# Performance work log

Hardware: AMD Instinct MI355X
Metric: run time of the kernel (lower is better)

Reference implementation:

```python
import jax, jax.numpy as jnp
import numpy as np

DIM = 768
NUM_HEADS = 12
HEAD_DIM = DIM // NUM_HEADS
TIME_STEPS = 4
TAU_MEM = 2.0
THRESH = 1.0
NOISE_PROB = 0.01


def setup_inputs() -> dict:
    key = jax.random.key(0)
    ks = jax.random.split(key, 9)
    B, N = 8, 1024
    s = 1.0 / np.sqrt(DIM)
    inp = {"x": jax.random.normal(ks[0], (B, N, DIM), jnp.float32)}
    for i, nm in enumerate(["q", "k", "v", "o"]):
        inp["W" + nm] = jax.random.normal(ks[1 + i], (DIM, DIM), jnp.float32) * s
        inp["b" + nm] = jax.random.normal(ks[5 + i], (DIM,), jnp.float32) * 0.01
    return inp


def _lif_spikes(inp):
    """Multi-step LIF: constant input each step, leaky integrate, hard threshold,
    soft reset; aggregated spikes clamped to 1 (binary). Straight-through sigmoid
    surrogate keeps the op differentiable without changing forward values."""
    decay = jnp.exp(jnp.asarray(-1.0 / TAU_MEM, inp.dtype))

    def step(v, _):
        v = v * decay + inp
        sur = jax.nn.sigmoid(4.0 * (v - THRESH))
        hard = (v >= THRESH).astype(inp.dtype)
        spike = jax.lax.stop_gradient(hard - sur) + sur
        v = v - THRESH * spike
        return v, spike

    _, spikes = jax.lax.scan(step, jnp.zeros_like(inp), None, length=TIME_STEPS)
    # sum over time then clamp(max=1.0) -> binary aggregate spike map
    return jnp.minimum(spikes.sum(axis=0), 1.0)


def reference(x, Wq, bq, Wk, bk, Wv, bv, Wo, bo):
    B, N, C = x.shape
    q_lin = x @ Wq.T + bq
    k_lin = x @ Wk.T + bk
    v_lin = x @ Wv.T + bv

    s_q = _lif_spikes(q_lin)  # (B,N,C) binary
    s_k = _lif_spikes(k_lin)
    s_v = _lif_spikes(v_lin)

    # noise injection for fully-silent samples (deterministic key)
    silent = jnp.all(s_q == 0, axis=(1, 2)) & jnp.all(s_k == 0, axis=(1, 2))  # (B,)
    nk = jax.random.split(jax.random.key(42), 2)
    noise_q = (jax.random.uniform(nk[0], s_q.shape) < NOISE_PROB).astype(s_q.dtype)
    noise_k = (jax.random.uniform(nk[1], s_k.shape) < NOISE_PROB).astype(s_k.dtype)
    s_q = jnp.where(silent[:, None, None], jnp.maximum(s_q, noise_q), s_q)
    s_k = jnp.where(silent[:, None, None], jnp.maximum(s_k, noise_k), s_k)

    # (B,H,N,Dh)
    s_q = s_q.reshape(B, N, NUM_HEADS, HEAD_DIM).transpose(0, 2, 1, 3)
    s_k = s_k.reshape(B, N, NUM_HEADS, HEAD_DIM).transpose(0, 2, 1, 3)
    s_v = s_v.reshape(B, N, NUM_HEADS, HEAD_DIM).transpose(0, 2, 1, 3)

    # XNOR similarity: sum_d (1 - (q-k)^2) = Dh - |q| - |k| + 2 q.k  (exact, since
    # the broadcast form expands to the same polynomial; q,k binary so q^2=q)
    q2 = jnp.sum(s_q * s_q, axis=-1)  # (B,H,N)
    k2 = jnp.sum(s_k * s_k, axis=-1)  # (B,H,N)
    qk = jnp.einsum('bhnd,bhmd->bhnm', s_q, s_k)
    scores = HEAD_DIM - q2[..., :, None] - k2[..., None, :] + 2.0 * qk  # (B,H,N,N)

    attn = jax.nn.sigmoid(scores)
    out = jnp.einsum('bhnm,bhmd->bhnd', attn, s_v)  # (B,H,N,Dh)
    out = out.transpose(0, 2, 1, 3).reshape(B, N, C)
    return out @ Wo.T + bo
```

## Files before the change

kernel.cpp:

```cpp
#include <hip/hip_runtime.h>


typedef __attribute__((ext_vector_type(8))) short short8;
typedef __attribute__((ext_vector_type(4))) float f32x4;
typedef unsigned long long u64;

static __device__ __forceinline__ unsigned short f2bf(float f) {
  unsigned int u = __builtin_bit_cast(unsigned int, f);
  return (unsigned short)((u + 0x7FFFu + ((u >> 16) & 1u)) >> 16);
}

static __device__ __forceinline__ u64 pack4bf(float a, float b, float c, float d) {
  return (u64)f2bf(a) | ((u64)f2bf(b) << 16) | ((u64)f2bf(c) << 32) |
         ((u64)f2bf(d) << 48);
}

static __device__ __forceinline__ void gl2lds16(const unsigned short* g,
                                                unsigned short* l) {
  __builtin_amdgcn_global_load_lds(
      (const __attribute__((address_space(1))) unsigned int*)(g),
      (__attribute__((address_space(3))) unsigned int*)(l),
      16, 0, 0);
}

__global__ void k_convert(const float* __restrict__ x,
                          const float* __restrict__ Wq, const float* __restrict__ bq,
                          const float* __restrict__ Wk, const float* __restrict__ bk,
                          const float* __restrict__ Wv, const float* __restrict__ bv,
                          unsigned short* __restrict__ xb,
                          unsigned short* __restrict__ wcat,
                          float* __restrict__ bcat,
                          int* __restrict__ cnt,
                          float* __restrict__ colsum) {
  const int X4 = 1572864;
  const int W4 = 147456;
  const int NB = 576;
  const int NZ = 1536;
  const int total = X4 + 3 * W4 + NB + NZ;
  int t = blockIdx.x * blockDim.x + threadIdx.x;
  if (t >= total) return;
  if (t == 0) *cnt = 0;
  if (t < X4) {
    float4 v = ((const float4*)x)[t];
    *(u64*)(xb + 4 * (long)t) = pack4bf(v.x, v.y, v.z, v.w);
  } else if (t < X4 + 3 * W4) {
    int j = t - X4;
    const float* src = Wq;
    int jj = j;
    if (jj >= 2 * W4) { src = Wv; jj -= 2 * W4; }
    else if (jj >= W4) { src = Wk; jj -= W4; }
    float4 v = ((const float4*)src)[jj];
    *(u64*)(wcat + 4 * (long)j) = pack4bf(v.x, v.y, v.z, v.w);
  } else if (t < X4 + 3 * W4 + NB) {
    int j = t - (X4 + 3 * W4);
    int idx = j * 4;
    const float* src = bq;
    int ii = idx;
    if (ii >= 1536) { src = bv; ii -= 1536; }
    else if (ii >= 768) { src = bk; ii -= 768; }
    float4 v = *(const float4*)(src + ii);
    *(float4*)(bcat + idx) = v;
  } else {
    int j = t - (X4 + 3 * W4 + NB);
    float4 z = {0.f, 0.f, 0.f, 0.f};
    ((float4*)colsum)[j] = z;
  }
}

__global__ __launch_bounds__(256, 4)
void k_qkv(const unsigned short* __restrict__ xb,
           const unsigned short* __restrict__ wcat,
           const float* __restrict__ bcat,
           u64* __restrict__ bits3,
           float* __restrict__ colsum)
{
  __shared__ __align__(16) unsigned short lA[128 * 64];
  __shared__ __align__(16) unsigned short lB[128 * 64];
  const int tid = threadIdx.x;
  const int lane = tid & 63;
  const int wid = tid >> 6;
  const int wm = wid >> 1, wn = wid & 1;
  const int row0 = blockIdx.x * 128;
  const int col0 = blockIdx.y * 128;
  const int srow = lane >> 3;
  const int scol = (lane & 7) * 8;
  const int rr = lane & 15;
  const int g = lane >> 4;
  const int g8 = g * 8;

  const unsigned short* gA = xb + (long)(row0 + wid * 32 + srow) * 768 + scol;
  const unsigned short* gB = wcat + (long)(col0 + wid * 32 + srow) * 768 + scol;
  unsigned short* sA = &lA[(wid * 32 + srow) * 64 + scol];
  unsigned short* sB = &lB[(wid * 32 + srow) * 64 + scol];

  f32x4 acc[4][4] = {};

#pragma unroll 1
  for (int kt = 0; kt < 768; kt += 64) {
    __syncthreads();
#pragma unroll
    for (int s = 0; s < 4; ++s) {
      gl2lds16(gA + s * (8 * 768) + kt, sA + s * (8 * 64));
      gl2lds16(gB + s * (8 * 768) + kt, sB + s * (8 * 64));
    }
    __syncthreads();
#pragma unroll
    for (int kk = 0; kk < 2; ++kk) {
      const int ko = kk * 32 + g8;
      short8 af[4];
#pragma unroll
      for (int i = 0; i < 4; ++i)
        af[i] = *(const short8*)&lA[(wm * 64 + i * 16 + rr) * 64 + ko];
#pragma unroll
      for (int j = 0; j < 4; ++j) {
        const short8 bf = *(const short8*)&lB[(wn * 64 + j * 16 + rr) * 64 + ko];
#pragma unroll
        for (int i = 0; i < 4; ++i)
          acc[i][j] = __builtin_amdgcn_mfma_f32_16x16x32_bf16(af[i], bf, acc[i][j], 0, 0, 0);
      }
    }
  }

  const int mi = blockIdx.y / 6;
  const int h = 2 * (blockIdx.y - mi * 6) + wn;
  u64* bits = bits3 + (long)mi * 98304;
  const float C_LIF = 0.45505041f;
  float thr[4];
#pragma unroll
  for (int j = 0; j < 4; ++j) thr[j] = C_LIF - bcat[col0 + wn * 64 + j * 16 + rr];

  float csum[4] = {0.f, 0.f, 0.f, 0.f};
#pragma unroll
  for (int i = 0; i < 4; ++i) {
#pragma unroll
    for (int r = 0; r < 4; ++r) {
      u64 map = 0;
#pragma unroll
      for (int j = 0; j < 4; ++j) {
        const bool sp = acc[i][j][r] >= thr[j];
        const u64 bl = __ballot(sp);
        map |= ((bl >> (g * 16)) & 0xFFFFull) << (j * 16);
        csum[j] += sp ? 1.0f : 0.0f;
      }
      if (rr == 0) {
        const int grow = row0 + wm * 64 + i * 16 + g * 4 + r;
        const int b = grow >> 10, n = grow & 1023;
        bits[((long)b * 12 + h) * 1024 + n] = map;
      }
    }
  }
  if (mi == 2) {
    const int b = row0 >> 10;
#pragma unroll
    for (int j = 0; j < 4; ++j) {
      float s = csum[j];
      s += __shfl_xor(s, 16);
      s += __shfl_xor(s, 32);
      if (lane < 16) atomicAdd(colsum + b * 768 + h * 64 + j * 16 + rr, s);
    }
  }
}

__global__ __launch_bounds__(256)
void k_sb(const u64* __restrict__ qbits, const u64* __restrict__ kbits,
          const float* __restrict__ colsum, const float* __restrict__ Wo,
          const float* __restrict__ bo,
          int* __restrict__ cnt, int4* __restrict__ list,
          float* __restrict__ base) {
  __shared__ __align__(16) u64 kb[1024];
  __shared__ u64 qs[128];
  __shared__ int pqv[128];
  __shared__ unsigned short ncList[128];
  __shared__ unsigned short kcList[1024];
  __shared__ int ncnt, kcnt;
  const int tid = threadIdx.x;
  const int bid = blockIdx.x;
  if (bid < 768) {
    const int bh = bid >> 3;
    const int ntile = (bid & 7) * 128;
    const u64* ksrc = kbits + (long)bh * 1024;
    const u64* qsrc = qbits + (long)bh * 1024 + ntile;
    if (tid == 0) { ncnt = 0; kcnt = 0; }
    __syncthreads();
#pragma unroll
    for (int u = 0; u < 4; ++u) {
      const int m = tid + 256 * u;
      const u64 v = ksrc[m];
      kb[m] = v;
      if (__popcll(v) >= 27) {
        const int p = atomicAdd(&kcnt, 1);
        kcList[p] = (unsigned short)m;
      }
    }
    if (tid < 128) {
      const u64 qv = qsrc[tid];
      qs[tid] = qv;
      const int pq = __popcll(qv);
      pqv[tid] = pq;
      if (pq >= 27) {
        const int p = atomicAdd(&ncnt, 1);
        ncList[p] = (unsigned short)tid;
      }
    }
    __syncthreads();
    const int nc = ncnt;
    for (int ii = 0; ii < nc; ++ii) {
      const int n = ncList[ii];
      const u64 qb = qs[n];
#pragma unroll
      for (int u = 0; u < 4; ++u) {
        const int m = tid + 256 * u;
        const int hd = __popcll(qb ^ kb[m]);
        if (hd > 52) {
          const int x = atomicAdd(cnt, 1);
          if (x < 8192) list[x] = make_int4(bh, ntile + n, m, hd);
        }
      }
    }
    const int kc = kcnt;
    const int n = tid >> 1;
    if (pqv[n] < 27) {
      const u64 qb = qs[n];
      for (int e = (tid & 1); e < kc; e += 2) {
        const int m = kcList[e];
        const int hd = __popcll(qb ^ kb[m]);
        if (hd > 52) {
          const int x = atomicAdd(cnt, 1);
          if (x < 8192) list[x] = make_int4(bh, ntile + n, m, hd);
        }
      }
    }
  } else {
    const int bb = bid - 768;
    const int b = bb / 3, ch = bb - b * 3;
    const int oc = ch * 256 + tid;
    const float4* c4 = (const float4*)(colsum + b * 768);
    const float4* w4 = (const float4*)(Wo + (long)oc * 768);
    float acc = bo[oc];
#pragma unroll 4
    for (int i = 0; i < 192; ++i) {
      const float4 c = c4[i], w = w4[i];
      acc += c.x * w.x + c.y * w.y + c.z * w.z + c.w * w.w;
    }
    base[b * 768 + oc] = acc;
  }
}

__global__ __launch_bounds__(192)
void k_out(const float* __restrict__ base, const int* __restrict__ cnt,
           const int4* __restrict__ list, const u64* __restrict__ vbits,
           const float* __restrict__ Wo, float* __restrict__ out) {
  const int row = blockIdx.x;
  const int b = row >> 10;
  float4 v = ((const float4*)(base + b * 768))[threadIdx.x];
  const int c = min(*cnt, 8192);
  if (c > 0) {
    const int n = row & 1023;
    for (int e = 0; e < c; ++e) {
      const int4 E = list[e];
      const int eb = E.x / 12;
      if (eb == b && E.y == n) {
        const int hh = E.x - eb * 12;
        const float s = (float)(64 - E.w);
        const float w = 1.0f / (1.0f + __expf(s));
        const u64 vb = vbits[(long)E.x * 1024 + E.z];
        float4 d = {0.f, 0.f, 0.f, 0.f};
        for (int dd = 0; dd < 64; ++dd)
          if ((vb >> dd) & 1ull) {
            const float* wp = Wo + (long)(threadIdx.x * 4) * 768 + hh * 64 + dd;
            d.x += wp[0]; d.y += wp[768]; d.z += wp[1536]; d.w += wp[2304];
          }
        v.x -= w * d.x; v.y -= w * d.y; v.z -= w * d.z; v.w -= w * d.w;
      }
    }
  }
  ((float4*)(out + (long)row * 768))[threadIdx.x] = v;
}

extern "C" void kernel_launch(void* const* d_in, const int* in_sizes, int n_in,
                              void* d_out, int out_size, void* d_ws, size_t ws_size,
                              hipStream_t stream) {
  const float* x  = (const float*)d_in[0];
  const float* Wq = (const float*)d_in[1];
  const float* bq = (const float*)d_in[2];
  const float* Wk = (const float*)d_in[3];
  const float* bk = (const float*)d_in[4];
  const float* Wv = (const float*)d_in[5];
  const float* bv = (const float*)d_in[6];
  const float* Wo = (const float*)d_in[7];
  const float* bo = (const float*)d_in[8];
  float* out = (float*)d_out;

  char* ws = (char*)d_ws;
  unsigned short* xb    = (unsigned short*)(ws + 0);
  unsigned short* wcat  = (unsigned short*)(ws + 12582912);
  float*          bcat  = (float*)(ws + 16121856);
  u64*            bits3 = (u64*)(ws + 16131072);
  float*          colsum = (float*)(ws + 18490368);
  float*          base   = (float*)(ws + 18514944);
  int*            cnt    = (int*)(ws + 18539520);
  int4*           list   = (int4*)(ws + 18539536);

  const u64* qbits = bits3;
  const u64* kbits = bits3 + 98304;
  const u64* vbits = bits3 + 2 * 98304;

  k_convert<<<dim3(7881), dim3(256), 0, stream>>>(x, Wq, bq, Wk, bk, Wv, bv,
                                                  xb, wcat, bcat, cnt, colsum);
  k_qkv<<<dim3(64, 18), dim3(256), 0, stream>>>(xb, wcat, bcat, bits3, colsum);
  k_sb<<<dim3(792), dim3(256), 0, stream>>>(qbits, kbits, colsum, Wo, bo,
                                            cnt, list, base);
  k_out<<<dim3(8192), dim3(192), 0, stream>>>(base, cnt, list, vbits, Wo, out);
}
```

Baseline: 87.92 us.

## Process each batch-head in one 1024-thread block for sparse score search

Restructures the sparse high-score pair search so each (batch, head) is handled by a single 1024-thread block instead of eight 256-thread blocks, one per 128-row query tile. Key bits are loaded and scanned for high-popcount entries once per head rather than eight times. The Wo·colsum base computation is remapped onto 1024-thread blocks. The grid shrinks from 792 to 102 blocks, which lowers parallelism and occupancy on a many-CU GPU, and the low-popcount query loop now runs its full candidate list in one thread rather than split across two.

New measurement: 177.3 us. 2.02x slower.

```diff
diff --git a/kernel.cpp b/kernel.cpp
--- a/kernel.cpp
+++ b/kernel.cpp
@@ -161,79 +161,60 @@
   }
 }
 
-__global__ __launch_bounds__(256)
+__global__ __launch_bounds__(1024)
 void k_sb(const u64* __restrict__ qbits, const u64* __restrict__ kbits,
           const float* __restrict__ colsum, const float* __restrict__ Wo,
           const float* __restrict__ bo,
           int* __restrict__ cnt, int4* __restrict__ list,
           float* __restrict__ base) {
   __shared__ __align__(16) u64 kb[1024];
-  __shared__ u64 qs[128];
-  __shared__ int pqv[128];
-  __shared__ unsigned short ncList[128];
+  __shared__ __align__(16) u64 qs[1024];
+  __shared__ unsigned short ncList[1024];
   __shared__ unsigned short kcList[1024];
   __shared__ int ncnt, kcnt;
   const int tid = threadIdx.x;
   const int bid = blockIdx.x;
-  if (bid < 768) {
-    const int bh = bid >> 3;
-    const int ntile = (bid & 7) * 128;
-    const u64* ksrc = kbits + (long)bh * 1024;
-    const u64* qsrc = qbits + (long)bh * 1024 + ntile;
+  if (bid < 96) {
+    const int bh = bid;
     if (tid == 0) { ncnt = 0; kcnt = 0; }
     __syncthreads();
-#pragma unroll
-    for (int u = 0; u < 4; ++u) {
-      const int m = tid + 256 * u;
-      const u64 v = ksrc[m];
-      kb[m] = v;
-      if (__popcll(v) >= 27) {
-        const int p = atomicAdd(&kcnt, 1);
-        kcList[p] = (unsigned short)m;
-      }
-    }
-    if (tid < 128) {
-      const u64 qv = qsrc[tid];
-      qs[tid] = qv;
-      const int pq = __popcll(qv);
-      pqv[tid] = pq;
-      if (pq >= 27) {
-        const int p = atomicAdd(&ncnt, 1);
-        ncList[p] = (unsigned short)tid;
-      }
+    const u64 kv = kbits[(long)bh * 1024 + tid];
+    kb[tid] = kv;
+    if (__popcll(kv) >= 27) {
+      const int p = atomicAdd(&kcnt, 1);
+      kcList[p] = (unsigned short)tid;
+    }
+    const u64 qv = qbits[(long)bh * 1024 + tid];
+    qs[tid] = qv;
+    const int pq = __popcll(qv);
+    if (pq >= 27) {
+      const int p = atomicAdd(&ncnt, 1);
+      ncList[p] = (unsigned short)tid;
     }
     __syncthreads();
     const int nc = ncnt;
     for (int ii = 0; ii < nc; ++ii) {
       const int n = ncList[ii];
-      const u64 qb = qs[n];
-#pragma unroll
-      for (int u = 0; u < 4; ++u) {
-        const int m = tid + 256 * u;
-        const int hd = __popcll(qb ^ kb[m]);
+      const int hd = __popcll(qs[n] ^ kb[tid]);
+      if (hd > 52) {
+        const int x = atomicAdd(cnt, 1);
+        if (x < 8192) list[x] = make_int4(bh, n, tid, hd);
+      }
+    }
+    if (pq < 27) {
+      const int kc = kcnt;
+      for (int e = 0; e < kc; ++e) {
+        const int m = kcList[e];
+        const int hd = __popcll(qv ^ kb[m]);
         if (hd > 52) {
           const int x = atomicAdd(cnt, 1);
-          if (x < 8192) list[x] = make_int4(bh, ntile + n, m, hd);
+          if (x < 8192) list[x] = make_int4(bh, tid, m, hd);
         }
       }
     }
-    const int kc = kcnt;
-    const int n = tid >> 1;
-    if (pqv[n] < 27) {
-      const u64 qb = qs[n];
-      for (int e = (tid & 1); e < kc; e += 2) {
-        const int m = kcList[e];
-        const int hd = __popcll(qb ^ kb[m]);
-        if (hd > 52) {
-          const int x = atomicAdd(cnt, 1);
-          if (x < 8192) list[x] = make_int4(bh, ntile + n, m, hd);
-        }
-      }
-    }
   } else {
-    const int bb = bid - 768;
-    const int b = bb / 3, ch = bb - b * 3;
-    const int oc = ch * 256 + tid;
+    const int idx = (bid - 96) * 1024 + tid;
+    const int b = idx / 768, oc = idx - b * 768;
     const float4* c4 = (const float4*)(colsum + b * 768);
     const float4* w4 = (const float4*)(Wo + (long)oc * 768);
     float acc = bo[oc];
@@ -308,7 +289,7 @@
   k_convert<<<dim3(7881), dim3(256), 0, stream>>>(x, Wq, bq, Wk, bk, Wv, bv,
                                                   xb, wcat, bcat, cnt, colsum);
   k_qkv<<<dim3(64, 18), dim3(256), 0, stream>>>(xb, wcat, bcat, bits3, colsum);
-  k_sb<<<dim3(792), dim3(256), 0, stream>>>(qbits, kbits, colsum, Wo, bo,
-                                            cnt, list, base);
+  k_sb<<<dim3(102), dim3(1024), 0, stream>>>(qbits, kbits, colsum, Wo, bo,
+                                             cnt, list, base);
   k_out<<<dim3(8192), dim3(192), 0, stream>>>(base, cnt, list, vbits, Wo, out);
 }
```
